# Performance work log

Hardware: AMD Instinct MI355X
Metric: run time of the kernel (lower is better)

## Reference

```python
import jax, jax.numpy as jnp
import numpy as np

N_NODES = 100000
N_EDGES = 3200000
IN_F = 128
HID = 128


def setup_inputs() -> dict:
    key = jax.random.key(0)
    ks = jax.random.split(key, 6)
    features = jax.random.normal(ks[0], (N_NODES, IN_F), dtype=jnp.float32)
    edge_index = jax.random.randint(ks[1], (2, N_EDGES), 0, N_NODES, dtype=jnp.int64)
    # Glorot-ish scaled weights
    W1 = jax.random.normal(ks[2], (IN_F, HID), dtype=jnp.float32) / np.sqrt(IN_F)
    b1 = jnp.zeros((HID,), dtype=jnp.float32)
    W2 = jax.random.normal(ks[3], (HID, HID), dtype=jnp.float32) / np.sqrt(HID)
    b2 = jnp.zeros((HID,), dtype=jnp.float32)
    prelu_a = jnp.full((HID,), 0.25, dtype=jnp.float32)  # nn.PReLU default init
    return {"features": features, "edge_index": edge_index,
            "W1": W1, "b1": b1, "W2": W2, "b2": b2, "prelu_a": prelu_a}


def _prelu(x, a):
    return jnp.where(x >= 0, x, a[None, :] * x)


def _graph_conv(x, W, b, a, src, dst, dout_is, din_is):
    # DGL GraphConv, norm='both': src-normalize, SpMM aggregate, dst-normalize,
    # dense transform, bias, activation.
    h = x * dout_is[:, None]                                   # [N, F]
    m = jax.ops.segment_sum(h[src], dst, num_segments=N_NODES)  # gather + scatter-add
    m = m * din_is[:, None]
    m = m @ W + b[None, :]
    return _prelu(m, a)


def reference(features, edge_index, W1, b1, W2, b2, prelu_a):
    src, dst = edge_index[0], edge_index[1]
    ones = jnp.ones((N_EDGES,), dtype=jnp.float32)
    deg_out = jax.ops.segment_sum(ones, src, num_segments=N_NODES)
    deg_in = jax.ops.segment_sum(ones, dst, num_segments=N_NODES)
    dout_is = jax.lax.rsqrt(jnp.clip(deg_out, 1.0))
    din_is = jax.lax.rsqrt(jnp.clip(deg_in, 1.0))
    h = _graph_conv(features, W1, b1, prelu_a, src, dst, dout_is, din_is)
    h = _graph_conv(h, W2, b2, prelu_a, src, dst, dout_is, din_is)
    return h
```

## Files before the change

### kernel.cpp

```cpp
#include <hip/hip_runtime.h>
#include <hip/hip_fp16.h>

#define NN 100000
#define EE 3200000
#define FF 128

#define NBUK 98
#define CH_A 8192
#define NB_A ((EE + CH_A - 1) / CH_A)

typedef _Float16 f16x8 __attribute__((ext_vector_type(8)));
typedef float f32x4 __attribute__((ext_vector_type(4)));

__global__ __launch_bounds__(256) void k_bukhist2(const int* __restrict__ ei,
                                                  int* __restrict__ dst_tot,
                                                  int* __restrict__ src_tot) {
  __shared__ int hd[NBUK];
  __shared__ int hs[NBUK];
  int tid = threadIdx.x;
  if (tid < NBUK) { hd[tid] = 0; hs[tid] = 0; }
  __syncthreads();
  int base = blockIdx.x * CH_A;
#pragma unroll
  for (int k = 0; k < CH_A / 256; ++k) {
    int e = base + k * 256 + tid;
    if (e < EE) {
      atomicAdd(&hs[ei[e] >> 10], 1);
      atomicAdd(&hd[ei[EE + e] >> 10], 1);
    }
  }
  __syncthreads();
  if (tid < NBUK) {
    if (hd[tid] > 0) atomicAdd(&dst_tot[tid], hd[tid]);
    if (hs[tid] > 0) atomicAdd(&src_tot[tid], hs[tid]);
  }
}

__global__ __launch_bounds__(64) void k_bukscan(const int* __restrict__ dst_tot,
                                                const int* __restrict__ src_tot,
                                                int* __restrict__ dbase,
                                                int* __restrict__ dcur,
                                                int* __restrict__ sbase,
                                                int* __restrict__ scur,
                                                int* __restrict__ offs) {
  if (threadIdx.x == 0) {
    int run = 0;
    for (int b = 0; b < NBUK; ++b) {
      dbase[b] = run; dcur[b] = run; run += dst_tot[b];
    }
    dbase[NBUK] = run;
    offs[NN] = run;
  }
  if (threadIdx.x == 1) {
    int run = 0;
    for (int b = 0; b < NBUK; ++b) {
      sbase[b] = run; scur[b] = run; run += src_tot[b];
    }
    sbase[NBUK] = run;
  }
}

__global__ __launch_bounds__(256) void k_bin2(const int* __restrict__ ei,
                                              int* __restrict__ dcur_g,
                                              int* __restrict__ scur_g,
                                              int2* __restrict__ binned,
                                              int* __restrict__ src_binned) {
  __shared__ int hd[NBUK];
  __shared__ int hs[NBUK];
  __shared__ int cd[NBUK];
  __shared__ int cs[NBUK];
  int tid = threadIdx.x;
  if (tid < NBUK) { hd[tid] = 0; hs[tid] = 0; }
  __syncthreads();
  int base = blockIdx.x * CH_A;
  const int* dst = ei + EE;
#pragma unroll
  for (int k = 0; k < CH_A / 256; ++k) {
    int e = base + k * 256 + tid;
    if (e < EE) {
      atomicAdd(&hs[ei[e] >> 10], 1);
      atomicAdd(&hd[dst[e] >> 10], 1);
    }
  }
  __syncthreads();
  if (tid < NBUK) {
    cd[tid] = (hd[tid] > 0) ? atomicAdd(&dcur_g[tid], hd[tid]) : 0;
    cs[tid] = (hs[tid] > 0) ? atomicAdd(&scur_g[tid], hs[tid]) : 0;
  }
  __syncthreads();
#pragma unroll
  for (int k = 0; k < CH_A / 256; ++k) {
    int e = base + k * 256 + tid;
    if (e < EE) {
      int s = ei[e];
      int d = dst[e];
      int dpos = atomicAdd(&cd[d >> 10], 1);
      binned[dpos] = make_int2(s, d);
      int spos = atomicAdd(&cs[s >> 10], 1);
      src_binned[spos] = s;
    }
  }
}

__global__ __launch_bounds__(1024) void k_csr(const int2* __restrict__ binned,
                                              const int* __restrict__ dbase,
                                              int* __restrict__ offs,
                                              float* __restrict__ din_is,
                                              int* __restrict__ csr_src) {
  __shared__ int h[1024];
  __shared__ int sa[1024];
  __shared__ int cur[1024];
  int tid = threadIdx.x;
  int b = blockIdx.x;
  int dst0 = b << 10;
  int beg = dbase[b];
  int cnt = dbase[b + 1] - beg;

  h[tid] = 0;
  __syncthreads();
  for (int t = tid; t < cnt; t += 1024) {
    atomicAdd(&h[binned[beg + t].y - dst0], 1);
  }
  __syncthreads();
  sa[tid] = h[tid];
  __syncthreads();
  for (int off = 1; off < 1024; off <<= 1) {
    int v = (tid >= off) ? sa[tid - off] : 0;
    __syncthreads();
    sa[tid] += v;
    __syncthreads();
  }
  int excl = sa[tid] - h[tid];
  cur[tid] = beg + excl;
  int node = dst0 + tid;
  if (node < NN) {
    offs[node] = beg + excl;
    int d = h[tid]; if (d < 1) d = 1;
    din_is[node] = rsqrtf((float)d);
  }
  __syncthreads();
  for (int t = tid; t < cnt; t += 1024) {
    int2 p = binned[beg + t];
    int pos = atomicAdd(&cur[p.y - dst0], 1);
    csr_src[pos] = p.x;
  }
}

__global__ __launch_bounds__(1024) void k_srchist(const int* __restrict__ src_binned,
                                                  const int* __restrict__ sbase,
                                                  float* __restrict__ dout_is) {
  __shared__ int h[1024];
  int tid = threadIdx.x;
  int b = blockIdx.x;
  int src0 = b << 10;
  int beg = sbase[b];
  int cnt = sbase[b + 1] - beg;
  h[tid] = 0;
  __syncthreads();
  for (int t = tid; t < cnt; t += 1024) {
    atomicAdd(&h[src_binned[beg + t] - src0], 1);
  }
  __syncthreads();
  int node = src0 + tid;
  if (node < NN) {
    int d = h[tid]; if (d < 1) d = 1;
    dout_is[node] = rsqrtf((float)d);
  }
}

__global__ __launch_bounds__(256) void k_wprep(const float* __restrict__ W,
                                               __half* __restrict__ Wt) {
  int t = blockIdx.x * blockDim.x + threadIdx.x;
  if (t >= FF * FF) return;
  int n = t >> 7, k = t & 127;
  Wt[n * FF + k] = __float2half(W[k * FF + n]);
}

__global__ __launch_bounds__(256) void k_prescale_h(const float* __restrict__ x,
                                                    const float* __restrict__ dout_is,
                                                    __half* __restrict__ xh) {
  int t = blockIdx.x * blockDim.x + threadIdx.x;
  if (t >= NN * (FF / 4)) return;
  int node = t >> 5;
  float sc = dout_is[node];
  float4 v = ((const float4*)x)[t];
  union { __half2 h[2]; uint2 u; } p;
  p.h[0] = __floats2half2_rn(v.x * sc, v.y * sc);
  p.h[1] = __floats2half2_rn(v.z * sc, v.w * sc);
  ((uint2*)xh)[t] = p.u;
}

__global__ __launch_bounds__(256) void k_agg(const __half* __restrict__ xh,
                                             const float* __restrict__ din_is,
                                             const int* __restrict__ offs,
                                             const int* __restrict__ csr_src,
                                             __half* __restrict__ outh) {
  int gid = blockIdx.x * blockDim.x + threadIdx.x;
  int node = gid >> 6;
  int lane = threadIdx.x & 63;
  if (node >= NN) return;
  int beg = offs[node], end = offs[node + 1];
  float ax = 0.f, ay = 0.f, bx = 0.f, by = 0.f;
  int e = beg;
  for (; e < end && (e & 3); ++e) {
    int s = csr_src[e];
    float2 v = __half22float2(((const __half2*)(xh + (size_t)s * FF))[lane]);
    ax += v.x; ay += v.y;
  }
  for (; e + 8 <= end; e += 8) {
    int4 i0 = *(const int4*)(csr_src + e);
    int4 i1 = *(const int4*)(csr_src + e + 4);
    float2 v0 = __half22float2(((const __half2*)(xh + (size_t)i0.x * FF))[lane]);
    float2 v1 = __half22float2(((const __half2*)(xh + (size_t)i0.y * FF))[lane]);
    float2 v2 = __half22float2(((const __half2*)(xh + (size_t)i0.z * FF))[lane]);
    float2 v3 = __half22float2(((const __half2*)(xh + (size_t)i0.w * FF))[lane]);
    float2 v4 = __half22float2(((const __half2*)(xh + (size_t)i1.x * FF))[lane]);
    float2 v5 = __half22float2(((const __half2*)(xh + (size_t)i1.y * FF))[lane]);
    float2 v6 = __half22float2(((const __half2*)(xh + (size_t)i1.z * FF))[lane]);
    float2 v7 = __half22float2(((const __half2*)(xh + (size_t)i1.w * FF))[lane]);
    ax += v0.x; ay += v0.y; bx += v1.x; by += v1.y;
    ax += v2.x; ay += v2.y; bx += v3.x; by += v3.y;
    ax += v4.x; ay += v4.y; bx += v5.x; by += v5.y;
    ax += v6.x; ay += v6.y; bx += v7.x; by += v7.y;
  }
  for (; e < end; ++e) {
    int s = csr_src[e];
    float2 v = __half22float2(((const __half2*)(xh + (size_t)s * FF))[lane]);
    ax += v.x; ay += v.y;
  }
  float di = din_is[node];
  __half2 r = __floats2half2_rn((ax + bx) * di, (ay + by) * di);
  ((__half2*)(outh + (size_t)node * FF))[lane] = r;
}

__global__ __launch_bounds__(256) void k_gemm_mfma(const __half* __restrict__ X,
                                                   const __half* __restrict__ Wt,
                                                   const float* __restrict__ bias,
                                                   const float* __restrict__ pa,
                                                   const float* __restrict__ postscale,
                                                   int out_half,
                                                   float* __restrict__ outf,
                                                   __half* __restrict__ outh) {
  __shared__ __half Xs[64][FF + 8];
  __shared__ __half Ws[FF][FF + 8];
  int tid = threadIdx.x;
  int row0 = blockIdx.x * 64;

  for (int t = tid; t < 64 * 16; t += 256) {
    int r = t >> 4, c8 = (t & 15) * 8;
    int row = row0 + r;
    uint4 v = make_uint4(0, 0, 0, 0);
    if (row < NN) v = *(const uint4*)(X + (size_t)row * FF + c8);
    *(uint4*)&Xs[r][c8] = v;
  }
  for (int t = tid; t < FF * 16; t += 256) {
    int r = t >> 4, c8 = (t & 15) * 8;
    uint4 v = *(const uint4*)(Wt + r * FF + c8);
    *(uint4*)&Ws[r][c8] = v;
  }
  __syncthreads();

  int wid = tid >> 6;
  int lane = tid & 63;
  int l15 = lane & 15;
  int g = lane >> 4;
  int arow = wid * 16 + l15;

  f32x4 acc[8];
#pragma unroll
  for (int n = 0; n < 8; ++n) acc[n] = (f32x4){0.f, 0.f, 0.f, 0.f};

  union FU { uint2 u[2]; f16x8 v; };
#pragma unroll
  for (int kk = 0; kk < 4; ++kk) {
    int kb = kk * 32;
    FU a;
    a.u[0] = *(const uint2*)&Xs[arow][kb + 4 * g];
    a.u[1] = *(const uint2*)&Xs[arow][kb + 16 + 4 * g];
#pragma unroll
    for (int n = 0; n < 8; ++n) {
      FU b;
      int wr = n * 16 + l15;
      b.u[0] = *(const uint2*)&Ws[wr][kb + 4 * g];
      b.u[1] = *(const uint2*)&Ws[wr][kb + 16 + 4 * g];
      acc[n] = __builtin_amdgcn_mfma_f32_16x16x32_f16(a.v, b.v, acc[n], 0, 0, 0);
    }
  }

#pragma unroll
  for (int n = 0; n < 8; ++n) {
    int col = n * 16 + l15;
    float bb = bias[col];
    float aa = pa[col];
#pragma unroll
    for (int j = 0; j < 4; ++j) {
      int row = row0 + wid * 16 + g * 4 + j;
      if (row < NN) {
        float v = acc[n][j] + bb;
        v = v >= 0.f ? v : aa * v;
        if (out_half) {
          v *= postscale[row];
          outh[(size_t)row * FF + col] = __float2half(v);
        } else {
          outf[(size_t)row * FF + col] = v;
        }
      }
    }
  }
}

extern "C" void kernel_launch(void* const* d_in, const int* in_sizes, int n_in,
                              void* d_out, int out_size, void* d_ws, size_t ws_size,
                              hipStream_t stream) {
  const float* features = (const float*)d_in[0];
  const int*   ei       = (const int*)d_in[1];
  const float* W1       = (const float*)d_in[2];
  const float* b1       = (const float*)d_in[3];
  const float* W2       = (const float*)d_in[4];
  const float* b2       = (const float*)d_in[5];
  const float* pa       = (const float*)d_in[6];
  float* out = (float*)d_out;

  char* ws = (char*)d_ws;
  size_t off = 0;
  auto alloc = [&](size_t bytes) -> void* {
    void* p = ws + off;
    off += (bytes + 255) & ~(size_t)255;
    return p;
  };
  int*    buk_tot = (int*)alloc((size_t)2 * NBUK * 4);
  int*    dst_tot = buk_tot;
  int*    src_tot = buk_tot + NBUK;
  float*  dout_is = (float*)alloc((size_t)NN * 4);
  float*  din_is  = (float*)alloc((size_t)NN * 4);
  int*    offs    = (int*)alloc((size_t)(NN + 1) * 4);
  int*    dbase   = (int*)alloc((size_t)(NBUK + 1) * 4);
  int*    dcur    = (int*)alloc((size_t)NBUK * 4);
  int*    sbase   = (int*)alloc((size_t)(NBUK + 1) * 4);
  int*    scur    = (int*)alloc((size_t)NBUK * 4);
  int*    csr_src = (int*)alloc((size_t)EE * 4);
  __half* tmp_h   = (__half*)alloc((size_t)EE * 8);
  __half* xh      = (__half*)alloc((size_t)NN * FF * 2);
  __half* w1t     = (__half*)alloc((size_t)FF * FF * 2);
  __half* w2t     = (__half*)alloc((size_t)FF * FF * 2);
  int2*   binned     = (int2*)tmp_h;
  int*    src_binned = (int*)xh;

  (void)hipMemsetAsync(buk_tot, 0, (size_t)2 * NBUK * 4, stream);

  k_bukhist2<<<NB_A, 256, 0, stream>>>(ei, dst_tot, src_tot);
  k_bukscan<<<1, 64, 0, stream>>>(dst_tot, src_tot, dbase, dcur, sbase, scur, offs);
  k_bin2<<<NB_A, 256, 0, stream>>>(ei, dcur, scur, binned, src_binned);
  k_csr<<<NBUK, 1024, 0, stream>>>(binned, dbase, offs, din_is, csr_src);
  k_srchist<<<NBUK, 1024, 0, stream>>>(src_binned, sbase, dout_is);

  k_wprep<<<(FF * FF + 255) / 256, 256, 0, stream>>>(W1, w1t);
  k_wprep<<<(FF * FF + 255) / 256, 256, 0, stream>>>(W2, w2t);

  k_prescale_h<<<(NN * FF / 4 + 255) / 256, 256, 0, stream>>>(features, dout_is, xh);
  k_agg<<<NN / 4, 256, 0, stream>>>(xh, din_is, offs, csr_src, tmp_h);
  k_gemm_mfma<<<(NN + 63) / 64, 256, 0, stream>>>(tmp_h, w1t, b1, pa, dout_is, 1, nullptr, xh);

  k_agg<<<NN / 4, 256, 0, stream>>>(xh, din_is, offs, csr_src, tmp_h);
  k_gemm_mfma<<<(NN + 63) / 64, 256, 0, stream>>>(tmp_h, w2t, b2, pa, nullptr, 0, out, nullptr);
}
```

Measured before the change: 472.8 us.

## Use fixed-capacity buckets to drop histogram pass and sort CSR neighbors by source range

Replaces the two-pass bucketing (global histogram, scan, then scatter) with a single scatter into fixed-capacity per-bucket slots of 256 nodes, so the separate histogram and scan kernels are removed. The CSR build now sub-sorts each destination's neighbor list into 8 source-id ranges, which should make the aggregation gathers more cache-local. Offsets become begin/end pairs because buckets are no longer contiguous. The cost is a larger workspace, and correctness relies on no 256-node bucket receiving more than CAP edges, which only holds for near-uniform random graphs.

```diff
diff --git a/kernel.cpp b/kernel.cpp
--- a/kernel.cpp
+++ b/kernel.cpp
@@ -5,72 +5,26 @@
 #define EE 3200000
 #define FF 128
 
-#define NBUK 98
+#define NBUK 391
+#define CAP 12288
 #define CH_A 8192
 #define NB_A ((EE + CH_A - 1) / CH_A)
+#define NCH 8
 
 typedef _Float16 f16x8 __attribute__((ext_vector_type(8)));
 typedef float f32x4 __attribute__((ext_vector_type(4)));
 
-__global__ __launch_bounds__(256) void k_bukhist2(const int* __restrict__ ei,
-                                                  int* __restrict__ dst_tot,
-                                                  int* __restrict__ src_tot) {
-  __shared__ int hd[NBUK];
-  __shared__ int hs[NBUK];
-  int tid = threadIdx.x;
-  if (tid < NBUK) { hd[tid] = 0; hs[tid] = 0; }
-  __syncthreads();
-  int base = blockIdx.x * CH_A;
-#pragma unroll
-  for (int k = 0; k < CH_A / 256; ++k) {
-    int e = base + k * 256 + tid;
-    if (e < EE) {
-      atomicAdd(&hs[ei[e] >> 10], 1);
-      atomicAdd(&hd[ei[EE + e] >> 10], 1);
-    }
-  }
-  __syncthreads();
-  if (tid < NBUK) {
-    if (hd[tid] > 0) atomicAdd(&dst_tot[tid], hd[tid]);
-    if (hs[tid] > 0) atomicAdd(&src_tot[tid], hs[tid]);
-  }
-}
-
-__global__ __launch_bounds__(64) void k_bukscan(const int* __restrict__ dst_tot,
-                                                const int* __restrict__ src_tot,
-                                                int* __restrict__ dbase,
-                                                int* __restrict__ dcur,
-                                                int* __restrict__ sbase,
-                                                int* __restrict__ scur,
-                                                int* __restrict__ offs) {
-  if (threadIdx.x == 0) {
-    int run = 0;
-    for (int b = 0; b < NBUK; ++b) {
-      dbase[b] = run; dcur[b] = run; run += dst_tot[b];
-    }
-    dbase[NBUK] = run;
-    offs[NN] = run;
-  }
-  if (threadIdx.x == 1) {
-    int run = 0;
-    for (int b = 0; b < NBUK; ++b) {
-      sbase[b] = run; scur[b] = run; run += src_tot[b];
-    }
-    sbase[NBUK] = run;
-  }
-}
-
-__global__ __launch_bounds__(256) void k_bin2(const int* __restrict__ ei,
-                                              int* __restrict__ dcur_g,
-                                              int* __restrict__ scur_g,
-                                              int2* __restrict__ binned,
-                                              int* __restrict__ src_binned) {
+__global__ __launch_bounds__(256) void k_bin(const int* __restrict__ ei,
+                                             int* __restrict__ dcur_g,
+                                             int* __restrict__ scur_g,
+                                             int2* __restrict__ binned,
+                                             int* __restrict__ src_binned) {
   __shared__ int hd[NBUK];
   __shared__ int hs[NBUK];
   __shared__ int cd[NBUK];
   __shared__ int cs[NBUK];
   int tid = threadIdx.x;
-  if (tid < NBUK) { hd[tid] = 0; hs[tid] = 0; }
+  for (int t = tid; t < NBUK; t += 256) { hd[t] = 0; hs[t] = 0; }
   __syncthreads();
   int base = blockIdx.x * CH_A;
   const int* dst = ei + EE;
@@ -78,14 +32,14 @@
   for (int k = 0; k < CH_A / 256; ++k) {
     int e = base + k * 256 + tid;
     if (e < EE) {
-      atomicAdd(&hs[ei[e] >> 10], 1);
-      atomicAdd(&hd[dst[e] >> 10], 1);
+      atomicAdd(&hs[ei[e] >> 8], 1);
+      atomicAdd(&hd[dst[e] >> 8], 1);
     }
   }
   __syncthreads();
-  if (tid < NBUK) {
-    cd[tid] = (hd[tid] > 0) ? atomicAdd(&dcur_g[tid], hd[tid]) : 0;
-    cs[tid] = (hs[tid] > 0) ? atomicAdd(&scur_g[tid], hs[tid]) : 0;
+  for (int t = tid; t < NBUK; t += 256) {
+    cd[t] = (hd[t] > 0) ? atomicAdd(&dcur_g[t], hd[t]) : 0;
+    cs[t] = (hs[t] > 0) ? atomicAdd(&scur_g[t], hs[t]) : 0;
   }
   __syncthreads();
 #pragma unroll
@@ -94,71 +48,82 @@
     if (e < EE) {
       int s = ei[e];
       int d = dst[e];
-      int dpos = atomicAdd(&cd[d >> 10], 1);
-      binned[dpos] = make_int2(s, d);
-      int spos = atomicAdd(&cs[s >> 10], 1);
-      src_binned[spos] = s;
+      int db = d >> 8;
+      int dpos = atomicAdd(&cd[db], 1);
+      binned[(size_t)db * CAP + dpos] = make_int2(s, d);
+      int sb = s >> 8;
+      int spos = atomicAdd(&cs[sb], 1);
+      src_binned[(size_t)sb * CAP + spos] = s;
     }
   }
 }
 
-__global__ __launch_bounds__(1024) void k_csr(const int2* __restrict__ binned,
-                                              const int* __restrict__ dbase,
-                                              int* __restrict__ offs,
-                                              float* __restrict__ din_is,
-                                              int* __restrict__ csr_src) {
-  __shared__ int h[1024];
-  __shared__ int sa[1024];
-  __shared__ int cur[1024];
+__global__ __launch_bounds__(256) void k_csr(const int2* __restrict__ binned,
+                                             const int* __restrict__ dcnt,
+                                             int2* __restrict__ offs2,
+                                             float* __restrict__ din_is,
+                                             int* __restrict__ csr_src) {
+  __shared__ int h2[256 * NCH];
+  __shared__ int sa[256];
+  __shared__ int cur2[256 * NCH];
   int tid = threadIdx.x;
   int b = blockIdx.x;
-  int dst0 = b << 10;
-  int beg = dbase[b];
-  int cnt = dbase[b + 1] - beg;
-
-  h[tid] = 0;
-  __syncthreads();
-  for (int t = tid; t < cnt; t += 1024) {
-    atomicAdd(&h[binned[beg + t].y - dst0], 1);
-  }
-  __syncthreads();
-  sa[tid] = h[tid];
-  __syncthreads();
-  for (int off = 1; off < 1024; off <<= 1) {
+  int dst0 = b << 8;
+  int gbeg = b * CAP;
+  int cnt = dcnt[b];
+
+#pragma unroll
+  for (int i = 0; i < NCH; ++i) h2[tid * NCH + i] = 0;
+  __syncthreads();
+  for (int t = tid; t < cnt; t += 256) {
+    int2 p = binned[gbeg + t];
+    int c = (unsigned)p.x / 12500u;
+    atomicAdd(&h2[(p.y - dst0) * NCH + c], 1);
+  }
+  __syncthreads();
+  int deg = 0;
+#pragma unroll
+  for (int i = 0; i < NCH; ++i) deg += h2[tid * NCH + i];
+  sa[tid] = deg;
+  __syncthreads();
+  for (int off = 1; off < 256; off <<= 1) {
     int v = (tid >= off) ? sa[tid - off] : 0;
     __syncthreads();
     sa[tid] += v;
     __syncthreads();
   }
-  int excl = sa[tid] - h[tid];
-  cur[tid] = beg + excl;
+  int excl = sa[tid] - deg;
+  int run = gbeg + excl;
+#pragma unroll
+  for (int i = 0; i < NCH; ++i) { cur2[tid * NCH + i] = run; run += h2[tid * NCH + i]; }
   int node = dst0 + tid;
   if (node < NN) {
-    offs[node] = beg + excl;
-    int d = h[tid]; if (d < 1) d = 1;
+    offs2[node] = make_int2(gbeg + excl, gbeg + excl + deg);
+    int d = deg < 1 ? 1 : deg;
     din_is[node] = rsqrtf((float)d);
   }
   __syncthreads();
-  for (int t = tid; t < cnt; t += 1024) {
-    int2 p = binned[beg + t];
-    int pos = atomicAdd(&cur[p.y - dst0], 1);
+  for (int t = tid; t < cnt; t += 256) {
+    int2 p = binned[gbeg + t];
+    int c = (unsigned)p.x / 12500u;
+    int pos = atomicAdd(&cur2[(p.y - dst0) * NCH + c], 1);
     csr_src[pos] = p.x;
   }
 }
 
-__global__ __launch_bounds__(1024) void k_srchist(const int* __restrict__ src_binned,
-                                                  const int* __restrict__ sbase,
-                                                  float* __restrict__ dout_is) {
-  __shared__ int h[1024];
+__global__ __launch_bounds__(256) void k_srchist(const int* __restrict__ src_binned,
+                                                 const int* __restrict__ scnt,
+                                                 float* __restrict__ dout_is) {
+  __shared__ int h[256];
   int tid = threadIdx.x;
   int b = blockIdx.x;
-  int src0 = b << 10;
-  int beg = sbase[b];
-  int cnt = sbase[b + 1] - beg;
+  int src0 = b << 8;
+  int gbeg = b * CAP;
+  int cnt = scnt[b];
   h[tid] = 0;
   __syncthreads();
-  for (int t = tid; t < cnt; t += 1024) {
-    atomicAdd(&h[src_binned[beg + t] - src0], 1);
+  for (int t = tid; t < cnt; t += 256) {
+    atomicAdd(&h[src_binned[gbeg + t] - src0], 1);
   }
   __syncthreads();
   int node = src0 + tid;
@@ -192,14 +157,15 @@
 
 __global__ __launch_bounds__(256) void k_agg(const __half* __restrict__ xh,
                                              const float* __restrict__ din_is,
-                                             const int* __restrict__ offs,
+                                             const int2* __restrict__ offs2,
                                              const int* __restrict__ csr_src,
                                              __half* __restrict__ outh) {
   int gid = blockIdx.x * blockDim.x + threadIdx.x;
   int node = gid >> 6;
   int lane = threadIdx.x & 63;
   if (node >= NN) return;
-  int beg = offs[node], end = offs[node + 1];
+  int2 oo = offs2[node];
+  int beg = oo.x, end = oo.y;
   float ax = 0.f, ay = 0.f, bx = 0.f, by = 0.f;
   int e = beg;
   for (; e < end && (e & 3); ++e) {
@@ -328,39 +294,33 @@
     off += (bytes + 255) & ~(size_t)255;
     return p;
   };
-  int*    buk_tot = (int*)alloc((size_t)2 * NBUK * 4);
-  int*    dst_tot = buk_tot;
-  int*    src_tot = buk_tot + NBUK;
+  int*    cur     = (int*)alloc((size_t)2 * NBUK * 4);
+  int*    dcur    = cur;
+  int*    scur    = cur + NBUK;
   float*  dout_is = (float*)alloc((size_t)NN * 4);
   float*  din_is  = (float*)alloc((size_t)NN * 4);
-  int*    offs    = (int*)alloc((size_t)(NN + 1) * 4);
-  int*    dbase   = (int*)alloc((size_t)(NBUK + 1) * 4);
-  int*    dcur    = (int*)alloc((size_t)NBUK * 4);
-  int*    sbase   = (int*)alloc((size_t)(NBUK + 1) * 4);
-  int*    scur    = (int*)alloc((size_t)NBUK * 4);
-  int*    csr_src = (int*)alloc((size_t)EE * 4);
-  __half* tmp_h   = (__half*)alloc((size_t)EE * 8);
-  __half* xh      = (__half*)alloc((size_t)NN * FF * 2);
+  int2*   offs2   = (int2*)alloc((size_t)NN * 8);
+  int*    csr_src = (int*)alloc((size_t)NBUK * CAP * 4);
+  int2*   binned  = (int2*)alloc((size_t)NBUK * CAP * 8);
+  int*    src_binned = (int*)alloc((size_t)NBUK * CAP * 4);
+  __half* tmp_h   = (__half*)alloc((size_t)NN * FF * 2);
   __half* w1t     = (__half*)alloc((size_t)FF * FF * 2);
   __half* w2t     = (__half*)alloc((size_t)FF * FF * 2);
-  int2*   binned     = (int2*)tmp_h;
-  int*    src_binned = (int*)xh;
-
-  (void)hipMemsetAsync(buk_tot, 0, (size_t)2 * NBUK * 4, stream);
-
-  k_bukhist2<<<NB_A, 256, 0, stream>>>(ei, dst_tot, src_tot);
-  k_bukscan<<<1, 64, 0, stream>>>(dst_tot, src_tot, dbase, dcur, sbase, scur, offs);
-  k_bin2<<<NB_A, 256, 0, stream>>>(ei, dcur, scur, binned, src_binned);
-  k_csr<<<NBUK, 1024, 0, stream>>>(binned, dbase, offs, din_is, csr_src);
-  k_srchist<<<NBUK, 1024, 0, stream>>>(src_binned, sbase, dout_is);
+  __half* xh      = (__half*)binned;
+
+  (void)hipMemsetAsync(cur, 0, (size_t)2 * NBUK * 4, stream);
+
+  k_bin<<<NB_A, 256, 0, stream>>>(ei, dcur, scur, binned, src_binned);
+  k_csr<<<NBUK, 256, 0, stream>>>(binned, dcur, offs2, din_is, csr_src);
+  k_srchist<<<NBUK, 256, 0, stream>>>(src_binned, scur, dout_is);
 
   k_wprep<<<(FF * FF + 255) / 256, 256, 0, stream>>>(W1, w1t);
   k_wprep<<<(FF * FF + 255) / 256, 256, 0, stream>>>(W2, w2t);
 
   k_prescale_h<<<(NN * FF / 4 + 255) / 256, 256, 0, stream>>>(features, dout_is, xh);
-  k_agg<<<NN / 4, 256, 0, stream>>>(xh, din_is, offs, csr_src, tmp_h);
+  k_agg<<<NN / 4, 256, 0, stream>>>(xh, din_is, offs2, csr_src, tmp_h);
   k_gemm_mfma<<<(NN + 63) / 64, 256, 0, stream>>>(tmp_h, w1t, b1, pa, dout_is, 1, nullptr, xh);
 
-  k_agg<<<NN / 4, 256, 0, stream>>>(xh, din_is, offs, csr_src, tmp_h);
+  k_agg<<<NN / 4, 256, 0, stream>>>(xh, din_is, offs2, csr_src, tmp_h);
   k_gemm_mfma<<<(NN + 63) / 64, 256, 0, stream>>>(tmp_h, w2t, b2, pa, nullptr, 0, out, nullptr);
 }
```

Measured after the change: 450.3 us. 1.05x faster.
